# Kernel tuning notes

Hardware: AMD Instinct MI355X
Metric: run time of the kernel (lower is better)

Reference implementation:

```python
import jax, jax.numpy as jnp
import numpy as np

SEQ_LEN, PRED_LEN = 512, 96
D_MODEL, D_STATE, D_FF = 512, 16, 512
DT_RANK = 32  # ceil(d_model / 16)
E_LAYERS = 2
B, N = 32, 256


def _layernorm(x, g, b, eps=1e-5):
    mu = jnp.mean(x, -1, keepdims=True)
    var = jnp.mean((x - mu) ** 2, -1, keepdims=True)
    return (x - mu) * jax.lax.rsqrt(var + eps) * g + b


def _mamba(x, win, convw, convb, wx, wdt, bdt, alog, dparam, wout):
    # x: [B, T, D] with T = n_variates + 6 (inverted tokens)
    Bb, T, D = x.shape
    xz = x @ win.T                      # [B, T, 2D] (expand=1 -> d_inner = D)
    xr, z = xz[..., :D], xz[..., D:]
    # causal depthwise conv, d_conv=2: y[t] = w0*x[t-1] + w1*x[t] + b
    x_prev = jnp.pad(xr, ((0, 0), (1, 0), (0, 0)))[:, :T]
    xc = jax.nn.silu(x_prev * convw[:, 0] + xr * convw[:, 1] + convb)
    dbl = xc @ wx.T                     # [B, T, dt_rank + 2*d_state]
    dt = jax.nn.softplus(dbl[..., :DT_RANK] @ wdt.T + bdt)     # [B, T, D]
    Bm = dbl[..., DT_RANK:DT_RANK + D_STATE]                    # [B, T, S]
    Cm = dbl[..., DT_RANK + D_STATE:]                           # [B, T, S]
    A = -jnp.exp(alog)                                          # [D, S]
    dA = jnp.exp(dt[..., None] * A)                             # [B, T, D, S]
    dBx = dt[..., None] * Bm[:, :, None, :] * xc[..., None]     # [B, T, D, S]

    def step(h, inp):
        a_t, bx_t = inp
        h = a_t * h + bx_t
        return h, h

    h0 = jnp.zeros((Bb, D, D_STATE), x.dtype)
    _, hs = jax.lax.scan(step, h0, (jnp.swapaxes(dA, 0, 1), jnp.swapaxes(dBx, 0, 1)))
    y = jnp.einsum('tbds,bts->btd', hs, Cm) + dparam * xc
    y = y * jax.nn.silu(z)
    return y @ wout.T


def _forward(x_enc, x_mark_enc, emb_w, emb_b, m_win, m_convw, m_convb, m_wx, m_wdt,
             m_bdt, m_alog, m_dparam, m_wout, ln1_g, ln1_b, ff1_w, ff1_b, ff2_w,
             ff2_b, ln2_g, ln2_b, lnf_g, lnf_b, proj_w, proj_b):
    n_var = x_enc.shape[2]
    # instance norm over time (use_norm=True)
    means = jnp.mean(x_enc, 1, keepdims=True)
    xn = x_enc - means
    stdev = jnp.sqrt(jnp.var(xn, axis=1, keepdims=True) + 1e-5)
    xn = xn / stdev
    # inverted embedding: tokens = variates (+ time-feature channels), proj seq_len -> d_model
    tok = jnp.concatenate([jnp.swapaxes(xn, 1, 2), jnp.swapaxes(x_mark_enc, 1, 2)], axis=1)
    h = tok @ emb_w.T + emb_b           # [B, n_var+6, d_model]
    for l in range(E_LAYERS):
        f = _mamba(h, m_win[l, 0], m_convw[l, 0], m_convb[l, 0], m_wx[l, 0],
                   m_wdt[l, 0], m_bdt[l, 0], m_alog[l, 0], m_dparam[l, 0], m_wout[l, 0])
        r = jnp.flip(_mamba(jnp.flip(h, 1), m_win[l, 1], m_convw[l, 1], m_convb[l, 1],
                            m_wx[l, 1], m_wdt[l, 1], m_bdt[l, 1], m_alog[l, 1],
                            m_dparam[l, 1], m_wout[l, 1]), 1)
        h = _layernorm(h + f + r, ln1_g[l], ln1_b[l])
        y = jax.nn.relu(h @ ff1_w[l].T + ff1_b[l]) @ ff2_w[l].T + ff2_b[l]
        h = _layernorm(h + y, ln2_g[l], ln2_b[l])
    h = _layernorm(h, lnf_g, lnf_b)
    dec = jnp.swapaxes(h @ proj_w.T + proj_b, 1, 2)[:, :, :n_var]  # [B, pred_len, N]
    dec = dec * stdev[:, 0, :][:, None, :] + means[:, 0, :][:, None, :]
    return dec


def setup_inputs() -> dict:
    key = jax.random.key(0)
    ks = iter(jax.random.split(key, 64))

    def rn(shape, scale=0.02):
        return jax.random.normal(next(ks), shape, dtype=jnp.float32) * scale

    D, S, R, L = D_MODEL, D_STATE, DT_RANK, E_LAYERS
    return dict(
        x_enc=jax.random.normal(next(ks), (B, SEQ_LEN, N), dtype=jnp.float32),
        x_mark_enc=jax.random.uniform(next(ks), (B, SEQ_LEN, 6), dtype=jnp.float32,
                                      minval=-1.0, maxval=1.0),
        emb_w=rn((D, SEQ_LEN)), emb_b=jnp.zeros((D,), jnp.float32),
        m_win=rn((L, 2, 2 * D, D)),
        m_convw=rn((L, 2, D, 2), 0.5),
        m_convb=jnp.zeros((L, 2, D), jnp.float32),
        m_wx=rn((L, 2, R + 2 * S, D)),
        m_wdt=rn((L, 2, D, R)),
        m_bdt=jnp.full((L, 2, D), -4.6, jnp.float32),  # softplus ~= 0.01
        m_alog=jnp.broadcast_to(jnp.log(jnp.arange(1, S + 1, dtype=jnp.float32)), (L, 2, D, S)) * jnp.ones((L, 2, D, S), jnp.float32),
        m_dparam=jnp.ones((L, 2, D), jnp.float32),
        m_wout=rn((L, 2, D, D)),
        ln1_g=jnp.ones((L, D), jnp.float32), ln1_b=jnp.zeros((L, D), jnp.float32),
        ff1_w=rn((L, D_FF, D)), ff1_b=jnp.zeros((L, D_FF), jnp.float32),
        ff2_w=rn((L, D, D_FF)), ff2_b=jnp.zeros((L, D), jnp.float32),
        ln2_g=jnp.ones((L, D), jnp.float32), ln2_b=jnp.zeros((L, D), jnp.float32),
        lnf_g=jnp.ones((D,), jnp.float32), lnf_b=jnp.zeros((D,), jnp.float32),
        proj_w=rn((PRED_LEN, D)), proj_b=jnp.zeros((PRED_LEN,), jnp.float32),
    )


def reference(x_enc, x_mark_enc, emb_w, emb_b, m_win, m_convw, m_convb, m_wx, m_wdt,
              m_bdt, m_alog, m_dparam, m_wout, ln1_g, ln1_b, ff1_w, ff1_b, ff2_w,
              ff2_b, ln2_g, ln2_b, lnf_g, lnf_b, proj_w, proj_b):
    return _forward(x_enc, x_mark_enc, emb_w, emb_b, m_win, m_convw, m_convb, m_wx,
                    m_wdt, m_bdt, m_alog, m_dparam, m_wout, ln1_g, ln1_b, ff1_w,
                    ff1_b, ff2_w, ff2_b, ln2_g, ln2_b, lnf_g, lnf_b, proj_w, proj_b)
```

## Files before the change

kernel.cpp:

```cpp
#include <hip/hip_runtime.h>
#include <hip/hip_bf16.h>
#include <math.h>
#include <stddef.h>

#define BB 32
#define TT 262
#define DD 512
#define SS 16
#define RR 32
#define SEQ 512
#define NV 256
#define PRED 96
#define MROWS (BB*TT)

typedef __attribute__((ext_vector_type(4))) float f32x4;
typedef __attribute__((ext_vector_type(8))) short s16x8;

__device__ inline ushort f2bu(float x) {
    __hip_bfloat16 h = __float2bfloat16(x);
    ushort u; __builtin_memcpy(&u, &h, 2); return u;
}
__device__ inline float bu2f(ushort u) {
    __hip_bfloat16 h; __builtin_memcpy(&h, &u, 2);
    return __bfloat162float(h);
}

__device__ inline void gload_lds16(const void* g, void* l) {
    __builtin_amdgcn_global_load_lds(
        (const __attribute__((address_space(1))) void*)g,
        (__attribute__((address_space(3))) void*)l, 16, 0, 0);
}

__global__ __launch_bounds__(256)
void packw(const float* __restrict__ in, ushort* __restrict__ out, int total)
{
    int idx = blockIdx.x * 256 + threadIdx.x;
    if (idx >= total) return;
    out[idx] = f2bu(in[idx]);
}

__global__ __launch_bounds__(256)
void mkcomb(const float* __restrict__ wx, const float* __restrict__ wdt,
            ushort* __restrict__ comb)
{
    int n  = blockIdx.x;
    int li = blockIdx.y;
    const float* wxl = wx + (size_t)li*64*512;
    ushort* outb = comb + ((size_t)li*544 + n)*512;
    if (n < 512) {
        __shared__ float wr[32];
        if (threadIdx.x < 32)
            wr[threadIdx.x] = wdt[(size_t)li*512*32 + (size_t)n*32 + threadIdx.x];
        __syncthreads();
        for (int kk = threadIdx.x; kk < 512; kk += 256) {
            float acc = 0.f;
            #pragma unroll
            for (int r = 0; r < 32; ++r)
                acc = fmaf(wr[r], wxl[r*512 + kk], acc);
            outb[kk] = f2bu(acc);
        }
    } else {
        int s = n - 512;
        for (int kk = threadIdx.x; kk < 512; kk += 256)
            outb[kk] = f2bu(wxl[(32+s)*512 + kk]);
    }
}

__global__ __launch_bounds__(256)
void stats_kernel(const float* __restrict__ x_enc,
                  float* __restrict__ mean, float* __restrict__ stdv)
{
    int b  = blockIdx.x >> 4;
    int n0 = (blockIdx.x & 15) << 4;
    int nl = threadIdx.x & 15;
    int tg = threadIdx.x >> 4;
    int n = n0 + nl;
    const float* base = x_enc + (size_t)b*SEQ*NV + n;
    float s0 = 0.f, s1 = 0.f, q0 = 0.f, q1 = 0.f;
    #pragma unroll 8
    for (int i = 0; i < 16; ++i) {
        int t = tg + i*32;
        float v0 = base[(size_t)t*NV];
        float v1 = base[(size_t)(t+16)*NV];
        s0 += v0; q0 = fmaf(v0, v0, q0);
        s1 += v1; q1 = fmaf(v1, v1, q1);
    }
    float s = s0 + s1, q = q0 + q1;
    __shared__ float ls[16][17], lq[16][17];
    ls[tg][nl] = s; lq[tg][nl] = q;
    __syncthreads();
    if (tg < 8) { ls[tg][nl] += ls[tg+8][nl]; lq[tg][nl] += lq[tg+8][nl]; }
    __syncthreads();
    if (tg < 4) { ls[tg][nl] += ls[tg+4][nl]; lq[tg][nl] += lq[tg+4][nl]; }
    __syncthreads();
    if (tg < 2) { ls[tg][nl] += ls[tg+2][nl]; lq[tg][nl] += lq[tg+2][nl]; }
    __syncthreads();
    if (tg == 0) {
        s = ls[0][nl] + ls[1][nl];
        q = lq[0][nl] + lq[1][nl];
        float mu  = s * (1.f/SEQ);
        float var = q * (1.f/SEQ) - mu*mu;
        mean[b*NV + n] = mu;
        stdv[b*NV + n] = sqrtf(var + 1e-5f);
    }
}

__global__ __launch_bounds__(256)
void tok_kernel(const float* __restrict__ x_enc, const float* __restrict__ x_mark,
                const float* __restrict__ mean, const float* __restrict__ stdv,
                ushort* __restrict__ tokb)
{
    int b  = blockIdx.x / 40;
    int r  = blockIdx.x % 40;
    int tt = r / 5;
    int vt = r % 5;
    int t0 = tt << 6, v0 = vt << 6;
    __shared__ float tile[64][65];
    int lv = threadIdx.x & 63;
    for (int i = threadIdx.x >> 6; i < 64; i += 4) {
        int t = t0 + i, v = v0 + lv;
        float val = 0.f;
        if (v < NV) {
            val = (x_enc[((size_t)b*SEQ + t)*NV + v] - mean[b*NV + v]) / stdv[b*NV + v];
        } else if (v < TT) {
            val = x_mark[((size_t)b*SEQ + t)*6 + (v - NV)];
        }
        tile[i][lv] = val;
    }
    __syncthreads();
    for (int i = threadIdx.x >> 6; i < 64; i += 4) {
        int v = v0 + i;
        if (v < TT) {
            size_t row = (size_t)b*TT + v;
            tokb[row*512 + t0 + lv] = f2bu(tile[lv][i]);
        }
    }
}

template<int HAS_BIAS, int RELU, int WF32, int W3, int SCANEP>
__global__ __launch_bounds__(256)
void gemm3(const ushort* __restrict__ A3, int lda3,
           const ushort* __restrict__ W3p, int ldw3,
           const float* __restrict__ bias,
           float* __restrict__ C, int ldc,
           ushort* __restrict__ C3, int N_out,
           float* __restrict__ bcbuf,
           size_t aOff, size_t wOff, size_t biasOff, size_t cOff, size_t bcOff,
           int M, int Nn, int K3)
{
    const int dir = blockIdx.y;
    A3  += (size_t)dir * aOff;
    W3p += (size_t)dir * wOff;
    if (HAS_BIAS || SCANEP) bias += (size_t)dir * biasOff;
    if (WF32) C += (size_t)dir * cOff;
    if (W3 || SCANEP) C3 += (size_t)dir * cOff;
    if (SCANEP) bcbuf += (size_t)dir * bcOff;

    __shared__ ushort lds[2][192*64];
    const int tid  = threadIdx.x;
    const int lane = tid & 63;
    const int wid  = tid >> 6;
    const int wr = wid >> 1, wc = wid & 1;

    int nwg = gridDim.x;
    int q8 = nwg >> 3, r8 = nwg & 7;
    int xcd = blockIdx.x & 7;
    int idx = blockIdx.x >> 3;
    int swz = (xcd < r8 ? xcd*(q8+1) : r8*(q8+1) + (xcd-r8)*q8) + idx;
    int ntile = (Nn + 63) >> 6;
    const int m0 = (swz / ntile) * 128;
    const int n0 = (swz % ntile) * 64;

    const int l8 = lane >> 3;
    const int sl = lane & 7;
    const int ssl = sl ^ l8;

    int arow[4], wrow[2];
    #pragma unroll
    for (int qq = 0; qq < 4; ++qq) {
        int r = (wid*4 + qq)*8 + l8;
        int ar = m0 + r; if (ar > M-1) ar = M-1;
        arow[qq] = ar;
    }
    #pragma unroll
    for (int qq = 0; qq < 2; ++qq) {
        int r = (wid*2 + qq)*8 + l8;
        int wrr = n0 + r; if (wrr > Nn-1) wrr = Nn-1;
        wrow[qq] = wrr;
    }

    f32x4 acc[4][2];
    #pragma unroll
    for (int i = 0; i < 4; ++i)
        #pragma unroll
        for (int j = 0; j < 2; ++j) acc[i][j] = (f32x4){0.f,0.f,0.f,0.f};

    const int nk = K3 >> 6;
    const int rl = lane & 15;
    const int kq = lane >> 4;

    auto stage = [&](int buf_, int kt_) {
        #pragma unroll
        for (int qq = 0; qq < 4; ++qq) {
            int c = wid*4 + qq;
            gload_lds16(A3 + (size_t)arow[qq]*lda3 + kt_*64 + ssl*8,
                        (void*)&lds[buf_][c*512]);
        }
        #pragma unroll
        for (int qq = 0; qq < 2; ++qq) {
            int c = wid*2 + qq;
            gload_lds16(W3p + (size_t)wrow[qq]*ldw3 + kt_*64 + ssl*8,
                        (void*)&lds[buf_][8192 + c*512]);
        }
    };

    stage(0, 0);
    __syncthreads();

    for (int kt = 0; kt < nk; ++kt) {
        int cur = kt & 1;
        if (kt + 1 < nk) stage(cur ^ 1, kt + 1);
        #pragma unroll
        for (int kk = 0; kk < 2; ++kk) {
            s16x8 av[4], wv[2];
            #pragma unroll
            for (int mi = 0; mi < 4; ++mi) {
                int row = wr*64 + mi*16 + rl;
                int ck = (kk*4 + kq) ^ (row & 7);
                av[mi] = *(const s16x8*)&lds[cur][row*64 + (ck<<3)];
            }
            #pragma unroll
            for (int ni = 0; ni < 2; ++ni) {
                int row = wc*32 + ni*16 + rl;
                int ck = (kk*4 + kq) ^ (row & 7);
                wv[ni] = *(const s16x8*)&lds[cur][8192 + row*64 + (ck<<3)];
            }
            #pragma unroll
            for (int mi = 0; mi < 4; ++mi)
                #pragma unroll
                for (int ni = 0; ni < 2; ++ni)
                    acc[mi][ni] = __builtin_amdgcn_mfma_f32_16x16x32_bf16(
                        av[mi], wv[ni], acc[mi][ni], 0, 0, 0);
        }
        __syncthreads();
    }

    #pragma unroll
    for (int ni = 0; ni < 2; ++ni) {
        int n = n0 + wc*32 + ni*16 + rl;
        if (n >= Nn) continue;
        float bv = (HAS_BIAS && !SCANEP) ? bias[n] : 0.f;
        #pragma unroll
        for (int mi = 0; mi < 4; ++mi) {
            #pragma unroll
            for (int j = 0; j < 4; ++j) {
                int m = m0 + wr*64 + mi*16 + kq*4 + j;
                if (m >= M) continue;
                float v = acc[mi][ni][j];
                if (SCANEP) {
                    if (n < 512) {
                        v += bias[n];
                        v = fmaxf(v, 0.f) + log1pf(__expf(-fabsf(v)));
                        C3[(size_t)m*ldc + n] = f2bu(v);
                    } else {
                        bcbuf[(size_t)m*N_out + (n - 512)] = v;
                    }
                } else {
                    if (HAS_BIAS) v += bv;
                    if (RELU) v = fmaxf(v, 0.f);
                    if (WF32) C[(size_t)m*ldc + n] = v;
                    if (W3)   C3[(size_t)m*N_out + n] = f2bu(v);
                }
            }
        }
    }
}

__global__ __launch_bounds__(256)
void conv2(ushort* __restrict__ xzb, const float* __restrict__ cwB,
           const float* __restrict__ cbB, float* __restrict__ xc,
           ushort* __restrict__ xcb)
{
    int gid = blockIdx.x * 256 + threadIdx.x;
    int d = gid & 511;
    int r = gid >> 9;
    int dir = (r >= MROWS) ? 1 : 0;
    int bt = r - dir*MROWS;
    int t = bt % TT;
    const float* cw = cwB + dir*DD*2;
    const float* cb = cbB + dir*DD;
    size_t base = (size_t)bt*2048 + (size_t)dir*1024;
    float cur = bu2f(xzb[base + d]);
    int tn = dir ? t + 1 : t - 1;
    float prev = 0.f;
    if (tn >= 0 && tn < TT)
        prev = bu2f(xzb[base + (dir ? 2048 : -2048) + d]);
    float v = prev*cw[d*2] + cur*cw[d*2+1] + cb[d];
    float sv = v / (1.f + __expf(-v));
    size_t o = (size_t)bt*1024 + dir*512 + d;
    xc[o] = sv;
    xcb[o] = f2bu(sv);
    float z = bu2f(xzb[base + 512 + d]);
    xzb[base + 512 + d] = f2bu(z / (1.f + __expf(-z)));
}

__global__ __launch_bounds__(256)
void scan_full(const ushort* __restrict__ sp_g, const float* __restrict__ xc_g,
               const ushort* __restrict__ xz_u, const float* __restrict__ bc_g,
               const float* __restrict__ alog, const float* __restrict__ dparam,
               ushort* __restrict__ yb)
{
    int dir = blockIdx.y;
    int rev = dir;
    sp_g += dir*512; xc_g += dir*512; bc_g += dir*32; xz_u += dir*1024;
    alog += (size_t)dir*DD*SS; dparam += (size_t)dir*DD;
    yb  += (size_t)dir*(size_t)MROWS*512;

    int sblk = blockIdx.x;
    int b  = sblk >> 4;
    int d0 = (sblk & 15) << 5;
    int tid = threadIdx.x;
    int sg = tid & 7;
    int dl = tid >> 3;
    int d  = d0 + dl;

    float Ac0 = -__expf(alog[d*SS + sg*2 + 0]);
    float Ac1 = -__expf(alog[d*SS + sg*2 + 1]);
    float dp = dparam[d];

    size_t bbase = (size_t)b*TT;
    size_t pstart = bbase + (rev ? TT-1 : 0);
    ptrdiff_t stp = rev ? -1 : 1;
    const ushort* spp = sp_g + pstart*1024 + d;
    const float*  xcp = xc_g + pstart*1024 + d;
    const ushort* zpp = xz_u + pstart*2048 + 512 + d;
    const float*  bcp = bc_g + pstart*64 + sg*2;
    ushort* ybp = yb + pstart*512 + d;
    const ptrdiff_t sp_s = stp*1024;
    const ptrdiff_t z_s  = stp*2048;
    const ptrdiff_t bc_s = stp*64;
    const ptrdiff_t yb_s = stp*512;

    float h0=0.f, h1=0.f;

    float sp_c = bu2f(*spp);
    float xc_c = *xcp;
    float z_c  = bu2f(*zpp);
    float2 B_c = *(const float2*)bcp;
    float2 C_c = *(const float2*)(bcp + 16);

    for (int t = 0; t < TT; ++t) {
        float sp_n = 0.f, xc_n = 0.f, z_n = 0.f;
        float2 B_n = {0,0}, C_n = {0,0};
        if (t + 1 < TT) {
            spp += sp_s; xcp += sp_s; zpp += z_s; bcp += bc_s;
            sp_n = bu2f(*spp);
            xc_n = *xcp;
            z_n  = bu2f(*zpp);
            B_n  = *(const float2*)bcp;
            C_n  = *(const float2*)(bcp + 16);
        }
        float dtxc = sp_c * xc_c;
        float e0 = __expf(sp_c*Ac0);
        float e1 = __expf(sp_c*Ac1);
        h0 = fmaf(e0, h0, dtxc*B_c.x);
        h1 = fmaf(e1, h1, dtxc*B_c.y);
        float dot = h0*C_c.x + h1*C_c.y;
        dot += __shfl_xor(dot, 1);
        dot += __shfl_xor(dot, 2);
        dot += __shfl_xor(dot, 4);
        if (sg == 0) {
            float yv = (dot + dp*xc_c) * z_c;
            *ybp = f2bu(yv);
        }
        ybp += yb_s;
        sp_c = sp_n; xc_c = xc_n; z_c = z_n; B_c = B_n; C_c = C_n;
    }
}

__global__ __launch_bounds__(64)
void ln_kernel(float* __restrict__ dst, const float* __restrict__ a,
               const float* __restrict__ b, const float* __restrict__ c,
               const float* __restrict__ g, const float* __restrict__ beta,
               ushort* __restrict__ outb)
{
    int row = blockIdx.x;
    int lane = threadIdx.x;
    size_t base = (size_t)row * DD;
    float x[8];
    #pragma unroll
    for (int j = 0; j < 2; ++j) {
        int e4 = j*64 + lane;
        float4 v = *(const float4*)(a + base + (size_t)e4*4);
        if (b) { float4 t = *(const float4*)(b + base + (size_t)e4*4); v.x+=t.x; v.y+=t.y; v.z+=t.z; v.w+=t.w; }
        if (c) { float4 t = *(const float4*)(c + base + (size_t)e4*4); v.x+=t.x; v.y+=t.y; v.z+=t.z; v.w+=t.w; }
        x[j*4+0]=v.x; x[j*4+1]=v.y; x[j*4+2]=v.z; x[j*4+3]=v.w;
    }
    float s = 0.f;
    #pragma unroll
    for (int i = 0; i < 8; ++i) s += x[i];
    #pragma unroll
    for (int m = 1; m < 64; m <<= 1) s += __shfl_xor(s, m);
    float mu = s * (1.f/DD);
    float vs = 0.f;
    #pragma unroll
    for (int i = 0; i < 8; ++i) { float dd = x[i]-mu; vs += dd*dd; }
    #pragma unroll
    for (int m = 1; m < 64; m <<= 1) vs += __shfl_xor(vs, m);
    float r = rsqrtf(vs*(1.f/DD) + 1e-5f);
    #pragma unroll
    for (int j = 0; j < 2; ++j) {
        int e4 = j*64 + lane;
        float4 gv = *(const float4*)(g    + (size_t)e4*4);
        float4 bv = *(const float4*)(beta + (size_t)e4*4);
        float4 o;
        o.x = (x[j*4+0]-mu)*r*gv.x + bv.x;
        o.y = (x[j*4+1]-mu)*r*gv.y + bv.y;
        o.z = (x[j*4+2]-mu)*r*gv.z + bv.z;
        o.w = (x[j*4+3]-mu)*r*gv.w + bv.w;
        *(float4*)(dst + base + (size_t)e4*4) = o;
        if (outb) {
            ushort* ob = outb + (size_t)row*512;
            ob[e4*4+0] = f2bu(o.x);
            ob[e4*4+1] = f2bu(o.y);
            ob[e4*4+2] = f2bu(o.z);
            ob[e4*4+3] = f2bu(o.w);
        }
    }
}

__global__ __launch_bounds__(256)
void proj_fin(const float* __restrict__ projtmp, const float* __restrict__ mean,
              const float* __restrict__ stdv, float* __restrict__ out)
{
    int b  = blockIdx.x >> 2;
    int n0 = (blockIdx.x & 3) << 6;
    __shared__ float tile[64][97];
    for (int i = threadIdx.x; i < 64*96; i += 256) {
        int rj = i / 96, cp = i % 96;
        tile[rj][cp] = projtmp[((size_t)b*TT + n0 + rj)*96 + cp];
    }
    __syncthreads();
    int nl = threadIdx.x & 63;
    int pg = threadIdx.x >> 6;
    int n = n0 + nl;
    float sd = stdv[b*NV + n];
    float mu = mean[b*NV + n];
    #pragma unroll
    for (int i = 0; i < 24; ++i) {
        int p = pg*24 + i;
        out[((size_t)b*PRED + p)*NV + n] = tile[nl][p]*sd + mu;
    }
}

extern "C" void kernel_launch(void* const* d_in, const int* in_sizes, int n_in,
                              void* d_out, int out_size, void* d_ws, size_t ws_size,
                              hipStream_t stream)
{
    (void)in_sizes; (void)n_in; (void)out_size; (void)ws_size;
    const float* x_enc   = (const float*)d_in[0];
    const float* x_mark  = (const float*)d_in[1];
    const float* emb_w   = (const float*)d_in[2];
    const float* emb_b   = (const float*)d_in[3];
    const float* m_win   = (const float*)d_in[4];
    const float* m_convw = (const float*)d_in[5];
    const float* m_convb = (const float*)d_in[6];
    const float* m_wx    = (const float*)d_in[7];
    const float* m_wdt   = (const float*)d_in[8];
    const float* m_bdt   = (const float*)d_in[9];
    const float* m_alog  = (const float*)d_in[10];
    const float* m_dpar  = (const float*)d_in[11];
    const float* m_wout  = (const float*)d_in[12];
    const float* ln1_g   = (const float*)d_in[13];
    const float* ln1_b   = (const float*)d_in[14];
    const float* ff1_w   = (const float*)d_in[15];
    const float* ff1_b   = (const float*)d_in[16];
    const float* ff2_w   = (const float*)d_in[17];
    const float* ff2_b   = (const float*)d_in[18];
    const float* ln2_g   = (const float*)d_in[19];
    const float* ln2_b   = (const float*)d_in[20];
    const float* lnf_g   = (const float*)d_in[21];
    const float* lnf_b   = (const float*)d_in[22];
    const float* proj_w  = (const float*)d_in[23];
    const float* proj_b  = (const float*)d_in[24];
    float* out = (float*)d_out;

    float* ws = (float*)d_ws;
    const size_t NBT = (size_t)MROWS;
    size_t off = 0;
    float* mean = ws + off; off += 8192;
    float* stdv = ws + off; off += 8192;
    ushort* w_emb  = (ushort*)(ws + off); off += 131072;
    ushort* w_win  = (ushort*)(ws + off); off += 1048576;
    ushort* w_wout = (ushort*)(ws + off); off += 524288;
    ushort* w_ff1  = (ushort*)(ws + off); off += 262144;
    ushort* w_ff2  = (ushort*)(ws + off); off += 262144;
    ushort* w_comb = (ushort*)(ws + off); off += 557056;
    ushort* w_proj = (ushort*)(ws + off); off += 24576;
    ushort* pool = (ushort*)(ws + off); off += NBT*768;
    ushort* tokb = pool;
    ushort* xcb  = pool;
    ushort* yb   = pool;
    float* h   = ws + off; off += NBT*512;
    ushort* hb = (ushort*)(ws + off); off += NBT*256;
    ushort* xzb = (ushort*)(ws + off); off += NBT*1024;
    ushort* fftb = xzb;
    ushort* spb = (ushort*)(ws + off); off += NBT*512;
    float* xcf = ws + off; off += NBT*1024;
    float* xs  = ws + off; off += NBT*512;
    float* bc2 = ws + off; off += NBT*64;
    float* fbuf = ws + off; off += NBT*512;
    float* rbuf = ws + off; off += NBT*512;
    float* projtmp = ws + off; off += NBT*96;
    (void)rbuf;

    packw<<<dim3((512*512+255)/256),  256, 0, stream>>>(emb_w, w_emb, 512*512);
    packw<<<dim3((4096*512+255)/256), 256, 0, stream>>>(m_win, w_win, 4096*512);
    packw<<<dim3((2048*512+255)/256), 256, 0, stream>>>(m_wout, w_wout, 2048*512);
    packw<<<dim3((1024*512+255)/256), 256, 0, stream>>>(ff1_w, w_ff1, 1024*512);
    packw<<<dim3((1024*512+255)/256), 256, 0, stream>>>(ff2_w, w_ff2, 1024*512);
    packw<<<dim3((96*512+255)/256),   256, 0, stream>>>(proj_w, w_proj, 96*512);
    mkcomb<<<dim3(544,4), 256, 0, stream>>>(m_wx, m_wdt, w_comb);

    stats_kernel<<<dim3(BB*16), 256, 0, stream>>>(x_enc, mean, stdv);
    tok_kernel<<<dim3(BB*40), 256, 0, stream>>>(x_enc, x_mark, mean, stdv, tokb);

    gemm3<1,0,1,1,0><<<dim3(66*8), 256, 0, stream>>>(tokb, 512, w_emb, 512,
        emb_b, h, DD, hb, 512, nullptr, 0,0,0,0,0, MROWS, 512, 512);

    for (int l = 0; l < 2; ++l) {
        gemm3<0,0,0,1,0><<<dim3(66*32), 256, 0, stream>>>(hb, 512,
            w_win + (size_t)l*2048*512, 512, nullptr,
            nullptr, 0, xzb, 2048, nullptr, 0,0,0,0,0, MROWS, 2048, 512);
        conv2<<<dim3((2*MROWS*DD)/256), 256, 0, stream>>>(xzb,
            m_convw + (size_t)l*2*DD*2, m_convb + (size_t)l*2*DD, xcf, xcb);
        gemm3<0,0,0,0,1><<<dim3(66*9, 2), 256, 0, stream>>>(
            xcb, 1024, w_comb + (size_t)l*2*544*512, 512,
            m_bdt + (size_t)l*2*DD, nullptr, 1024, spb, 64, bc2,
            512, (size_t)544*512, 512,
            512, 32, MROWS, 544, 512);
        const float* al = m_alog + (size_t)l*2*DD*SS;
        const float* dpp = m_dpar + (size_t)l*2*DD;
        scan_full<<<dim3(BB*16, 2), 256, 0, stream>>>(spb, xcf, xzb, bc2,
            al, dpp, yb);
        gemm3<0,0,1,0,0><<<dim3(66*8, 2), 256, 0, stream>>>(yb, 512,
            w_wout + (size_t)l*2*512*512, 512, nullptr,
            fbuf, DD, nullptr, 0, nullptr,
            NBT*512, (size_t)512*512, 0,
            NBT*512, 0, MROWS, 512, 512);
        ln_kernel<<<dim3(MROWS), 64, 0, stream>>>(h, h, fbuf, rbuf,
            ln1_g + l*DD, ln1_b + l*DD, hb);
        gemm3<1,1,0,1,0><<<dim3(66*8), 256, 0, stream>>>(hb, 512,
            w_ff1 + (size_t)l*512*512, 512, ff1_b + l*DD,
            nullptr, 0, fftb, 512, nullptr, 0,0,0,0,0, MROWS, 512, 512);
        gemm3<1,0,1,0,0><<<dim3(66*8), 256, 0, stream>>>(fftb, 512,
            w_ff2 + (size_t)l*512*512, 512, ff2_b + l*DD,
            xs, DD, nullptr, 0, nullptr, 0,0,0,0,0, MROWS, 512, 512);
        ln_kernel<<<dim3(MROWS), 64, 0, stream>>>(h, h, xs, nullptr,
            ln2_g + l*DD, ln2_b + l*DD, hb);
    }
    ln_kernel<<<dim3(MROWS), 64, 0, stream>>>(fbuf, h, nullptr, nullptr,
                                              lnf_g, lnf_b, hb);
    gemm3<1,0,1,0,0><<<dim3(66*2), 256, 0, stream>>>(hb, 512, w_proj, 512,
        proj_b, projtmp, 96, nullptr, 0, nullptr, 0,0,0,0,0, MROWS, 96, 512);
    proj_fin<<<dim3(BB*4), 256, 0, stream>>>(projtmp, mean, stdv, out);
}
```

Measured before the change: 685.4 us.

## Give each scan thread all 16 states of one channel, dropping shuffles

Reworks the selective-scan kernel so each thread owns one d channel and keeps all 16 state values in registers, instead of 8 threads sharing a channel with 2 states each. This removes the per-step cross-lane shuffle reduction and the single-writer predicate, and cuts the thread count 8x (512 single-wave blocks). The trade is far fewer waves to hide the latency of the serial recurrence and more registers per thread. B/C loads become wave-uniform broadcast vector loads.

Result: slower. 771.2 us (+12.5%).

```diff
diff --git a/kernel.cpp b/kernel.cpp
--- a/kernel.cpp
+++ b/kernel.cpp
@@ -304,7 +304,7 @@
     xzb[base + 512 + d] = f2bu(z / (1.f + __expf(-z)));
 }
 
-__global__ __launch_bounds__(256)
+__global__ __launch_bounds__(64)
 void scan_full(const ushort* __restrict__ sp_g, const float* __restrict__ xc_g,
                const ushort* __restrict__ xz_u, const float* __restrict__ bc_g,
                const float* __restrict__ alog, const float* __restrict__ dparam,
@@ -316,16 +316,13 @@
     alog += (size_t)dir*DD*SS; dparam += (size_t)dir*DD;
     yb  += (size_t)dir*(size_t)MROWS*512;
 
-    int sblk = blockIdx.x;
-    int b  = sblk >> 4;
-    int d0 = (sblk & 15) << 5;
-    int tid = threadIdx.x;
-    int sg = tid & 7;
-    int dl = tid >> 3;
-    int d  = d0 + dl;
-
-    float Ac0 = -__expf(alog[d*SS + sg*2 + 0]);
-    float Ac1 = -__expf(alog[d*SS + sg*2 + 1]);
+    int b  = blockIdx.x >> 3;
+    int d  = ((blockIdx.x & 7) << 6) + threadIdx.x;
+
+    float Ac[16];
+    #pragma unroll
+    for (int j = 0; j < 16; ++j)
+        Ac[j] = -__expf(alog[d*SS + j]);
     float dp = dparam[d];
 
     size_t bbase = (size_t)b*TT;
@@ -334,47 +331,64 @@
     const ushort* spp = sp_g + pstart*1024 + d;
     const float*  xcp = xc_g + pstart*1024 + d;
     const ushort* zpp = xz_u + pstart*2048 + 512 + d;
-    const float*  bcp = bc_g + pstart*64 + sg*2;
+    const float*  bcp = bc_g + pstart*64;
     ushort* ybp = yb + pstart*512 + d;
     const ptrdiff_t sp_s = stp*1024;
     const ptrdiff_t z_s  = stp*2048;
     const ptrdiff_t bc_s = stp*64;
     const ptrdiff_t yb_s = stp*512;
 
-    float h0=0.f, h1=0.f;
+    float h[16];
+    #pragma unroll
+    for (int j = 0; j < 16; ++j) h[j] = 0.f;
 
     float sp_c = bu2f(*spp);
     float xc_c = *xcp;
     float z_c  = bu2f(*zpp);
-    float2 B_c = *(const float2*)bcp;
-    float2 C_c = *(const float2*)(bcp + 16);
+    f32x4 B_c[4], C_c[4];
+    #pragma unroll
+    for (int q = 0; q < 4; ++q) {
+        B_c[q] = ((const f32x4*)bcp)[q];
+        C_c[q] = ((const f32x4*)(bcp + 16))[q];
+    }
 
     for (int t = 0; t < TT; ++t) {
         float sp_n = 0.f, xc_n = 0.f, z_n = 0.f;
-        float2 B_n = {0,0}, C_n = {0,0};
+        f32x4 B_n[4], C_n[4];
+        #pragma unroll
+        for (int q = 0; q < 4; ++q) { B_n[q] = (f32x4){0,0,0,0}; C_n[q] = (f32x4){0,0,0,0}; }
         if (t + 1 < TT) {
             spp += sp_s; xcp += sp_s; zpp += z_s; bcp += bc_s;
             sp_n = bu2f(*spp);
             xc_n = *xcp;
             z_n  = bu2f(*zpp);
-            B_n  = *(const float2*)bcp;
-            C_n  = *(const float2*)(bcp + 16);
+            #pragma unroll
+            for (int q = 0; q < 4; ++q) {
+                B_n[q] = ((const f32x4*)bcp)[q];
+                C_n[q] = ((const f32x4*)(bcp + 16))[q];
+            }
         }
         float dtxc = sp_c * xc_c;
-        float e0 = __expf(sp_c*Ac0);
-        float e1 = __expf(sp_c*Ac1);
-        h0 = fmaf(e0, h0, dtxc*B_c.x);
-        h1 = fmaf(e1, h1, dtxc*B_c.y);
-        float dot = h0*C_c.x + h1*C_c.y;
-        dot += __shfl_xor(dot, 1);
-        dot += __shfl_xor(dot, 2);
-        dot += __shfl_xor(dot, 4);
-        if (sg == 0) {
-            float yv = (dot + dp*xc_c) * z_c;
-            *ybp = f2bu(yv);
-        }
+        #pragma unroll
+        for (int j = 0; j < 16; ++j) {
+            float e = __expf(sp_c * Ac[j]);
+            h[j] = fmaf(e, h[j], dtxc * B_c[j >> 2][j & 3]);
+        }
+        float p0 = 0.f, p1 = 0.f, p2 = 0.f, p3 = 0.f;
+        #pragma unroll
+        for (int q = 0; q < 4; ++q) {
+            p0 = fmaf(h[q*4+0], C_c[q][0], p0);
+            p1 = fmaf(h[q*4+1], C_c[q][1], p1);
+            p2 = fmaf(h[q*4+2], C_c[q][2], p2);
+            p3 = fmaf(h[q*4+3], C_c[q][3], p3);
+        }
+        float dot = (p0 + p1) + (p2 + p3);
+        float yv = (dot + dp*xc_c) * z_c;
+        *ybp = f2bu(yv);
         ybp += yb_s;
-        sp_c = sp_n; xc_c = xc_n; z_c = z_n; B_c = B_n; C_c = C_n;
+        sp_c = sp_n; xc_c = xc_n; z_c = z_n;
+        #pragma unroll
+        for (int q = 0; q < 4; ++q) { B_c[q] = B_n[q]; C_c[q] = C_n[q]; }
     }
 }
 
@@ -541,7 +555,7 @@
             512, 32, MROWS, 544, 512);
         const float* al = m_alog + (size_t)l*2*DD*SS;
         const float* dpp = m_dpar + (size_t)l*2*DD;
-        scan_full<<<dim3(BB*16, 2), 256, 0, stream>>>(spb, xcf, xzb, bc2,
+        scan_full<<<dim3(BB*8, 2), 64, 0, stream>>>(spb, xcf, xzb, bc2,
             al, dpp, yb);
         gemm3<0,0,1,0,0><<<dim3(66*8, 2), 256, 0, stream>>>(yb, 512,
             w_wout + (size_t)l*2*512*512, 512, nullptr,
```
